# Optimization experiments

Measured on AMD Instinct MI355X. Metric: run time of the kernel, lower is better.

Reference implementation:

```python
import jax, jax.numpy as jnp
import numpy as np

MIN_NORM = 1e-15
EPS = 1e-7     # float32 eps used by the Hyperboloid manifold
MAX_NORM = 1e6

# ---- Hyperboloid (Lorentz) math, curvature c = k > 0, K = 1/k ----

def mink_dot(x, y):
    return jnp.sum(x * y, -1, keepdims=True) - 2.0 * x[..., :1] * y[..., :1]

def mink_norm(u):
    return jnp.sqrt(jnp.clip(mink_dot(u, u), EPS, None))

def proj(x, k):
    # project onto hyperboloid: x0 = sqrt(K + ||y||^2), spatial part kept
    K = 1.0 / k
    y = x[..., 1:]
    x0 = jnp.sqrt(jnp.clip(K + jnp.sum(y * y, -1, keepdims=True), EPS, None))
    return jnp.concatenate([x0, y], -1)

def proj_tan(u, x, k):
    ux = jnp.sum(x[..., 1:] * u[..., 1:], -1, keepdims=True)
    u0 = ux / jnp.clip(x[..., :1], EPS, None)
    return jnp.concatenate([u0 * jnp.ones_like(u[..., :1]), u[..., 1:]], -1)

def expmap(u, x, k):
    sqrtK = jnp.sqrt(1.0 / k)
    theta = jnp.clip(jnp.clip(mink_norm(u), None, MAX_NORM) / sqrtK, MIN_NORM, None)
    return proj(jnp.cosh(theta) * x + jnp.sinh(theta) * u / theta, k)

def expmap0(u, k):
    sqrtK = jnp.sqrt(1.0 / k)
    s = u[..., 1:]
    sn = jnp.clip(jnp.linalg.norm(s, axis=-1, keepdims=True), MIN_NORM, None)
    theta = sn / sqrtK
    out = jnp.concatenate([sqrtK * jnp.cosh(theta), sqrtK * jnp.sinh(theta) * s / sn], -1)
    return proj(out, k)

def logmap0(x, k):
    sqrtK = jnp.sqrt(1.0 / k)
    y = x[..., 1:]
    yn = jnp.clip(jnp.linalg.norm(y, axis=-1, keepdims=True), MIN_NORM, None)
    theta = jnp.clip(x[..., :1] / sqrtK, 1.0 + EPS, None)
    sp = sqrtK * jnp.arccosh(theta) * y / yn
    return jnp.concatenate([jnp.zeros_like(sp[..., :1]), sp], -1)

def ptransp0(x, u, k):
    sqrtK = jnp.sqrt(1.0 / k)
    x0, y = x[..., :1], x[..., 1:]
    yn = jnp.clip(jnp.linalg.norm(y, axis=-1, keepdims=True), MIN_NORM, None)
    yh = y / yn
    v = jnp.concatenate([-yn, (sqrtK - x0) * yh], -1)
    alpha = jnp.sum(yh * u[..., 1:], -1, keepdims=True) / sqrtK
    return proj_tan(u - alpha * v, x, k)

def mobius_matvec(m, x, k):
    return expmap0(logmap0(x, k) @ m.T, k)

def mobius_add(x, y, k):
    return expmap(ptransp0(x, logmap0(y, k), k), x, k)

def one_rnn_transform(W, h, U, x, b, k):
    Wh_Ux = mobius_add(mobius_matvec(W, h, k), mobius_matvec(U, x, k), k)
    return mobius_add(Wh_Ux, expmap0(b, k), k)

# ---- Mobius GRU cell (hyperbolic_hidden_state0=True, hyperbolic_input=False,
#      hyperbolic_output=True, nonlin=None) ----

def gru_cell(xt, hx, weight_ih, weight_hh, bias, k):
    # prepend zero time-coordinate and lift Euclidean input onto the hyperboloid
    xt = jnp.concatenate([jnp.zeros_like(xt[..., :1]), xt], -1)
    xt = expmap0(xt, k)
    W_ir, W_ih, W_iz = jnp.split(weight_ih, 3, axis=0)
    W_hr, W_hh, W_hz = jnp.split(weight_hh, 3, axis=0)
    b_r, b_h, b_z = bias[0:1], bias[1:2], bias[2:3]
    z_t = jax.nn.sigmoid(logmap0(one_rnn_transform(W_hz, hx, W_iz, xt, b_z, k), k))
    r_t = jax.nn.sigmoid(logmap0(one_rnn_transform(W_hr, hx, W_ir, xt, b_r, k), k))
    rh_t = expmap0(r_t * logmap0(hx, k), k)
    h_tilde = one_rnn_transform(W_hh, rh_t, W_ih, xt, b_h, k)
    delta_h = mobius_add(proj(-hx, k), h_tilde, k)
    h_int = ptransp0(hx, z_t * logmap0(delta_h, k), k)
    return expmap(h_int, hx, k)  # hyperbolic_output=True -> no final logmap0


def setup_inputs() -> dict:
    key = jax.random.key(0)
    k0, k1, k2, k3 = jax.random.split(key, 4)
    B, T, Din, H = 64, 512, 256, 256
    H1, D1 = H + 1, Din + 1
    stdv = 1.0 / np.sqrt(H1)
    x = 0.1 * jax.random.normal(k0, (B, T, Din), jnp.float32)
    weight_ih = jax.random.uniform(k1, (3 * H1, D1), jnp.float32, -stdv, stdv)
    weight_hh = jax.random.uniform(k2, (3 * H1, H1), jnp.float32, -stdv, stdv)
    bias = jnp.concatenate(
        [jnp.zeros((3, 1), jnp.float32), 1e-5 * jax.random.normal(k3, (3, H), jnp.float32)], -1)
    kk = jnp.ones((1,), jnp.float32)
    return {"x": x, "k": kk, "weight_ih": weight_ih, "weight_hh": weight_hh, "bias": bias}


def reference(x, k, weight_ih, weight_hh, bias):
    B = x.shape[0]
    H1 = weight_hh.shape[1]
    h0 = jnp.zeros((B, H1), x.dtype)  # default h0 (num_layers = 1)
    x_tm = jnp.swapaxes(x, 0, 1)  # [T, B, Din]

    def step(hx, xt):
        h = gru_cell(xt, hx, weight_ih, weight_hh, bias, k)
        return h, h

    h_last, outs = jax.lax.scan(step, h0, x_tm)  # outs: [T, B, H1]
    ht = h_last[..., 1:][None]  # drop time coord -> [1, B, H]
    return outs, ht
```

## Files before the change

### kernel.cpp

```cpp
#include <hip/hip_runtime.h>
#include <hip/hip_fp16.h>
#include <stdint.h>

#define B_  64
#define T_  512
#define H1_ 257

typedef _Float16 h2v __attribute__((ext_vector_type(2)));

__device__ __forceinline__ float frcp(float x) { return __builtin_amdgcn_rcpf(x); }
__device__ __forceinline__ float frsq(float x) { return __builtin_amdgcn_rsqf(x); }
__device__ __forceinline__ h2v u2h(uint32_t u) { return __builtin_bit_cast(h2v, u); }
__device__ __forceinline__ float fdot2(uint32_t a, uint32_t b, float c) {
  return __builtin_amdgcn_fdot2(u2h(a), u2h(b), c, false);
}
__device__ __forceinline__ uint32_t pkh(float a, float b) {
  __half2 h = __halves2half2(__float2half(a), __float2half(b));
  return __builtin_bit_cast(uint32_t, h);
}

#define LDS_BAR() do { \
  asm volatile("s_waitcnt lgkmcnt(0)" ::: "memory"); \
  __builtin_amdgcn_s_barrier(); \
  asm volatile("" ::: "memory"); \
} while (0)

template <int CTRL>
__device__ __forceinline__ float dpp_add(float v) {
  int t = __builtin_amdgcn_update_dpp(0, __builtin_bit_cast(int, v), CTRL, 0xf, 0xf, true);
  return v + __builtin_bit_cast(float, t);
}
__device__ __forceinline__ float wsum(float v) {
  v = dpp_add<0xB1>(v);  v = dpp_add<0x4E>(v);
  v = dpp_add<0x141>(v); v = dpp_add<0x140>(v);
  v = dpp_add<0x142>(v); v = dpp_add<0x143>(v);
  return __builtin_bit_cast(float, __builtin_amdgcn_readlane(__builtin_bit_cast(int, v), 63));
}
__device__ __forceinline__ void wsum2(float a, float b, float& ra, float& rb) {
  a = dpp_add<0xB1>(a);  b = dpp_add<0xB1>(b);
  a = dpp_add<0x4E>(a);  b = dpp_add<0x4E>(b);
  a = dpp_add<0x141>(a); b = dpp_add<0x141>(b);
  a = dpp_add<0x140>(a); b = dpp_add<0x140>(b);
  a = dpp_add<0x142>(a); b = dpp_add<0x142>(b);
  a = dpp_add<0x143>(a); b = dpp_add<0x143>(b);
  ra = __builtin_bit_cast(float, __builtin_amdgcn_readlane(__builtin_bit_cast(int, a), 63));
  rb = __builtin_bit_cast(float, __builtin_amdgcn_readlane(__builtin_bit_cast(int, b), 63));
}
__device__ __forceinline__ float sq4w(const float* s) {
  return wsum(s[0]*s[0] + s[1]*s[1] + s[2]*s[2] + s[3]*s[3]);
}
__device__ __forceinline__ float dot4w(const float* a, const float* b) {
  return wsum(a[0]*b[0] + a[1]*b[1] + a[2]*b[2] + a[3]*b[3]);
}

__device__ __forceinline__ float logc_(float x0, float ss, float sqrtK, float rsqK) {
  float yn = sqrtf(fmaxf(ss, 1e-30f));
  float th = fmaxf(x0 * rsqK, 1.0f + 1e-7f);
  float ac = __logf(th + sqrtf(th*th - 1.0f));
  return sqrtK * ac * frcp(yn);
}

__device__ __forceinline__ void madd_body(float* xs, float ss, float x0,
                                          const float* lm, float ssl, float dotXL,
                                          float K, float sqrtK, float rsqK) {
  float inv = frsq(fmaxf(ss, 1e-30f));
  float alpha = inv * dotXL * rsqK;
  float c2 = alpha * (sqrtK - x0);
  float ciw = c2 * inv;
  float ux = dotXL - ciw * ss;
  float w0 = ux * frcp(fmaxf(x0, 1e-7f));
  float ssw = fmaxf(ssl - 2.0f*ciw*dotXL + ciw*ciw*ss, 0.0f);
  float md = ssw - w0 * w0;
  float mn = sqrtf(fmaxf(md, 1e-7f));
  float th = fmaxf(fminf(mn, 1e6f) * rsqK, 1e-15f);
  float ex = __expf(th), ei = frcp(ex);
  float ch = 0.5f * (ex + ei);
  float sh = 0.5f * (ex - ei) * frcp(th);
  float A = ch - sh * ciw;
#pragma unroll
  for (int e = 0; e < 4; ++e) xs[e] = A * xs[e] + sh * lm[e];
}

__device__ __forceinline__ float madds_body(float* xs, float ss, float x0,
                                            const float* lm, float ssl, float dotXL,
                                            float sqrtK, float rsqK) {
  float inv = frsq(fmaxf(ss, 1e-30f));
  float alpha = inv * dotXL * rsqK;
  float c2 = alpha * (sqrtK - x0);
  float ciw = c2 * inv;
  float ux = dotXL - ciw * ss;
  float ssw = fmaxf(ssl - 2.0f*ciw*dotXL + ciw*ciw*ss, 0.0f);
  float nss = fmaxf(ss + 2.0f*ux + ssw, 0.0f);
  float Bc = 1.0f - ciw;
#pragma unroll
  for (int e = 0; e < 4; ++e) xs[e] = Bc * xs[e] + lm[e];
  return nss;
}

__device__ __forceinline__ void gate_chain(float* v, const float* lq, float ssl_q,
                                           const float* lmb, float ssl_b,
                                           float K, float sqrtK, float rsqK, float* sig) {
  float ssv, dvl;
  wsum2(v[0]*v[0]+v[1]*v[1]+v[2]*v[2]+v[3]*v[3],
        v[0]*lq[0]+v[1]*lq[1]+v[2]*lq[2]+v[3]*lq[3], ssv, dvl);
  float sn = sqrtf(fmaxf(ssv, 1e-30f));
  float th = sn * rsqK;
  float ex = __expf(th), ei = frcp(ex);
  float sh = 0.5f * (ex - ei);
  float ce = sqrtK * sh * frcp(sn);
#pragma unroll
  for (int e = 0; e < 4; ++e) v[e] = ce * v[e];
  float tq = sqrtK * sh;
  float ss = tq * tq;
  float x0 = sqrtf(fmaxf(K + ss, 1e-7f));
  madd_body(v, ss, x0, lq, ssl_q, ce * dvl, K, sqrtK, rsqK);
  float ssm, dbm;
  wsum2(v[0]*v[0]+v[1]*v[1]+v[2]*v[2]+v[3]*v[3],
        v[0]*lmb[0]+v[1]*lmb[1]+v[2]*lmb[2]+v[3]*lmb[3], ssm, dbm);
  float x0m = sqrtf(fmaxf(K + ssm, 1e-7f));
  float nss = madds_body(v, ssm, x0m, lmb, ssl_b, dbm, sqrtK, rsqK);
  float x0f = sqrtf(fmaxf(K + nss, 1e-7f));
  float c = logc_(x0f, nss, sqrtK, rsqK);
#pragma unroll
  for (int e = 0; e < 4; ++e) sig[e] = frcp(1.0f + __expf(-c * v[e]));
}

__global__ void pack_weights(const float* __restrict__ wih, const float* __restrict__ whh,
                             uint4* __restrict__ Pih, uint4* __restrict__ Phh) {
  int idx = blockIdx.x * 256 + threadIdx.x;
  int m   = idx / 24576;
  int rem = idx % 24576;
  int k4  = rem / 768;
  int col = rem % 768;
  int g   = col >> 8;
  int j   = col & 255;
  int gsrc = (g == 0) ? 2 : ((g == 1) ? 0 : 1);
  const float* src = (m == 0) ? wih : whh;
  const float* row = src + (size_t)(gsrc * H1_ + 1 + j) * H1_ + 1 + 8 * k4;
  uint4 o;
  o.x = pkh(row[0], row[1]);
  o.y = pkh(row[2], row[3]);
  o.z = pkh(row[4], row[5]);
  o.w = pkh(row[6], row[7]);
  ((m == 0) ? Pih : Phh)[(size_t)k4 * 768 + col] = o;
}

__global__ void precompute_xu(const float* __restrict__ x, const uint4* __restrict__ U4,
                              float* __restrict__ xU) {
  __shared__ __align__(16) uint32_t xp[8][128];
  const int tid = threadIdx.x;
  const int row0 = blockIdx.x * 8;
#pragma unroll
  for (int it = 0; it < 4; ++it) {
    int item = it * 256 + tid;
    int r = item >> 7, i = item & 127;
    int row = row0 + r;
    int t = row >> 6, bb = row & 63;
    const float* xr = x + ((size_t)bb * T_ + t) * 256;
    float2 xv = ((const float2*)xr)[i];
    xp[r][i] = pkh(xv.x, xv.y);
  }
  __syncthreads();
  float acc[8][3];
#pragma unroll
  for (int r = 0; r < 8; ++r)
#pragma unroll
    for (int c = 0; c < 3; ++c) acc[r][c] = 0.f;

#pragma unroll 2
  for (int k4 = 0; k4 < 32; ++k4) {
    uint4 w0 = U4[(size_t)k4 * 768 + tid];
    uint4 w1 = U4[(size_t)k4 * 768 + 256 + tid];
    uint4 w2 = U4[(size_t)k4 * 768 + 512 + tid];
#pragma unroll
    for (int r = 0; r < 8; ++r) {
      uint4 gp = ((const uint4*)xp[r])[k4];
      acc[r][0] = fdot2(w0.x, gp.x, acc[r][0]); acc[r][0] = fdot2(w0.y, gp.y, acc[r][0]);
      acc[r][0] = fdot2(w0.z, gp.z, acc[r][0]); acc[r][0] = fdot2(w0.w, gp.w, acc[r][0]);
      acc[r][1] = fdot2(w1.x, gp.x, acc[r][1]); acc[r][1] = fdot2(w1.y, gp.y, acc[r][1]);
      acc[r][1] = fdot2(w1.z, gp.z, acc[r][1]); acc[r][1] = fdot2(w1.w, gp.w, acc[r][1]);
      acc[r][2] = fdot2(w2.x, gp.x, acc[r][2]); acc[r][2] = fdot2(w2.y, gp.y, acc[r][2]);
      acc[r][2] = fdot2(w2.z, gp.z, acc[r][2]); acc[r][2] = fdot2(w2.w, gp.w, acc[r][2]);
    }
  }
#pragma unroll
  for (int r = 0; r < 8; ++r)
#pragma unroll
    for (int c = 0; c < 3; ++c)
      xU[(size_t)(row0 + r) * 768 + c * 256 + tid] = acc[r][c];
}

__global__ void xuss_kernel(const float* __restrict__ xU, float* __restrict__ xUss) {
  int row  = (blockIdx.x * 256 + threadIdx.x) >> 6;
  int lane = threadIdx.x & 63;
  const float4* base = (const float4*)(xU + (size_t)row * 768);
#pragma unroll
  for (int g = 0; g < 3; ++g) {
    float4 v = base[g * 64 + lane];
    float s = wsum(v.x*v.x + v.y*v.y + v.z*v.z + v.w*v.w);
    if (lane == 63) xUss[(size_t)row * 3 + g] = s;
  }
}

__global__ __launch_bounds__(512, 1) void mobius_gru_scan(
    const float* __restrict__ xU, const float* __restrict__ xUss,
    const uint4* __restrict__ W4, const float* __restrict__ bias,
    const float* __restrict__ kin, float* __restrict__ out) {
  __shared__ __align__(16) uint4 LWH[32][256];
  __shared__ __align__(16) uint32_t lds_gp[128];
  __shared__ __align__(16) float lds_v[512];
  __shared__ __align__(16) float lds_v2[512];
  __shared__ __align__(16) float lds_vh[512];
  __shared__ __align__(16) float lds_zg[256];

  const int tid  = threadIdx.x;
  const int lane = tid & 63;
  const int wave = tid >> 6;
  const int b    = blockIdx.x;
  const int j    = tid & 255;
  const int kh   = tid >> 8;

  const float kk    = kin[0];
  const float K     = 1.0f / kk;
  const float sqrtK = sqrtf(K);
  const float rsqK  = 1.0f / sqrtK;

#pragma unroll
  for (int it = 0; it < 16; ++it) {
    int idx = it * 512 + tid;
    int k4 = idx >> 8, jj = idx & 255;
    LWH[k4][jj] = W4[(size_t)k4 * 768 + 512 + jj];
  }

  uint4 vz[16], vr[16];
#pragma unroll
  for (int i = 0; i < 16; ++i) vz[i] = W4[(size_t)(kh * 16 + i) * 768 + j];
#pragma unroll
  for (int i = 0; i < 16; ++i) vr[i] = W4[(size_t)(kh * 16 + i) * 768 + 256 + j];
#pragma unroll
  for (int i = 0; i < 16; ++i) {
    asm volatile("" : "+v"(vz[i].x), "+v"(vz[i].y), "+v"(vz[i].z), "+v"(vz[i].w));
    asm volatile("" : "+v"(vr[i].x), "+v"(vr[i].y), "+v"(vr[i].z), "+v"(vr[i].w));
  }

  float lmeb[3][4]; float sslb[3];
  {
    const int rows[3] = {2, 0, 1};
#pragma unroll
    for (int g = 0; g < 3; ++g) {
#pragma unroll
      for (int e = 0; e < 4; ++e) lmeb[g][e] = bias[rows[g] * H1_ + 1 + 4 * lane + e];
      sslb[g] = sq4w(lmeb[g]);
    }
  }

  float h0c = 0.f, hs[4] = {0.f, 0.f, 0.f, 0.f}, ssh = 0.f;
  float gh[4] = {0.f, 0.f, 0.f, 0.f};

  float4 xvr_c = {0,0,0,0}, xvh_c = {0,0,0,0}, xvz_c = {0,0,0,0};
  float s0c = 0.f, s1c = 0.f, s2c = 0.f;
  if (wave == 0) {
    const float* xrow = xU + (size_t)b * 768;
    xvr_c = ((const float4*)(xrow + 256))[lane];
    xvh_c = ((const float4*)(xrow + 512))[lane];
    const float* srow = xUss + (size_t)b * 3;
    s1c = srow[1]; s2c = srow[2];
    uint2 p; p.x = 0u; p.y = 0u;
    ((uint2*)lds_gp)[lane] = p;
  } else if (wave == 1) {
    const float* xrow = xU + (size_t)b * 768;
    xvz_c = ((const float4*)xrow)[lane];
    s0c = xUss[(size_t)b * 3];
  }

  __syncthreads();

  for (int t = 0; t < T_; ++t) {
    if (t) LDS_BAR();

    {
      float a0 = 0.f, a1 = 0.f, a2 = 0.f, a3 = 0.f;
      float c0 = 0.f, c1 = 0.f, c2 = 0.f, c3 = 0.f;
#pragma unroll
      for (int i = 0; i < 16; ++i) {
        uint4 gp = ((const uint4*)lds_gp)[kh * 16 + i];
        a0 = fdot2(vr[i].x, gp.x, a0);
        a1 = fdot2(vr[i].y, gp.y, a1);
        a2 = fdot2(vr[i].z, gp.z, a2);
        a3 = fdot2(vr[i].w, gp.w, a3);
        c0 = fdot2(vz[i].x, gp.x, c0);
        c1 = fdot2(vz[i].y, gp.y, c1);
        c2 = fdot2(vz[i].z, gp.z, c2);
        c3 = fdot2(vz[i].w, gp.w, c3);
      }
      lds_v[kh * 256 + j]  = (a0 + a1) + (a2 + a3);
      lds_v2[kh * 256 + j] = (c0 + c1) + (c2 + c3);
    }
    float4 xvr_n = {0,0,0,0}, xvh_n = {0,0,0,0}, xvz_n = {0,0,0,0};
    float s0n = 0.f, s1n = 0.f, s2n = 0.f;
    if (t + 1 < T_) {
      if (wave == 0) {
        const float* nx = xU + (size_t)((t + 1) * B_ + b) * 768;
        xvr_n = ((const float4*)(nx + 256))[lane];
        xvh_n = ((const float4*)(nx + 512))[lane];
        const float* srow = xUss + (size_t)((t + 1) * B_ + b) * 3;
        s1n = srow[1]; s2n = srow[2];
      } else if (wave == 1) {
        const float* nx = xU + (size_t)((t + 1) * B_ + b) * 768;
        xvz_n = ((const float4*)nx)[lane];
        s0n = xUss[(size_t)((t + 1) * B_ + b) * 3];
      }
    }
    LDS_BAR();

    if (wave == 0) {
      float v[4], xv[4];
      {
        float4 pa = ((const float4*)lds_v)[lane];
        float4 pb = ((const float4*)lds_v)[64 + lane];
        v[0] = pa.x + pb.x; v[1] = pa.y + pb.y; v[2] = pa.z + pb.z; v[3] = pa.w + pb.w;
      }
      xv[0] = xvr_c.x; xv[1] = xvr_c.y; xv[2] = xvr_c.z; xv[3] = xvr_c.w;
      float rg[4];
      gate_chain(v, xv, s1c, lmeb[1], sslb[1], K, sqrtK, rsqK, rg);
      uint2 p;
      p.x = pkh(rg[0] * gh[0], rg[1] * gh[1]);
      p.y = pkh(rg[2] * gh[2], rg[3] * gh[3]);
      ((uint2*)lds_gp)[lane] = p;
    } else if (wave == 1) {
      float v[4], xv[4];
      {
        float4 pa = ((const float4*)lds_v2)[lane];
        float4 pb = ((const float4*)lds_v2)[64 + lane];
        v[0] = pa.x + pb.x; v[1] = pa.y + pb.y; v[2] = pa.z + pb.z; v[3] = pa.w + pb.w;
      }
      xv[0] = xvz_c.x; xv[1] = xvz_c.y; xv[2] = xvz_c.z; xv[3] = xvz_c.w;
      float zg[4];
      gate_chain(v, xv, s0c, lmeb[0], sslb[0], K, sqrtK, rsqK, zg);
      float4 z4 = {zg[0], zg[1], zg[2], zg[3]};
      ((float4*)lds_zg)[lane] = z4;
    }
    LDS_BAR();

    {
      const uint4* wl = &LWH[kh * 16][j];
      float a0 = 0.f, a1 = 0.f, a2 = 0.f, a3 = 0.f;
#pragma unroll
      for (int i = 0; i < 16; ++i) {
        uint4 w  = wl[(size_t)i * 256];
        uint4 gp = ((const uint4*)lds_gp)[kh * 16 + i];
        a0 = fdot2(w.x, gp.x, a0);
        a1 = fdot2(w.y, gp.y, a1);
        a2 = fdot2(w.z, gp.z, a2);
        a3 = fdot2(w.w, gp.w, a3);
      }
      lds_vh[kh * 256 + j] = (a0 + a1) + (a2 + a3);
    }
    LDS_BAR();

    if (wave == 0) {
      float4 z4 = ((const float4*)lds_zg)[lane];
      float4 pa = ((const float4*)lds_vh)[lane];
      float4 pb = ((const float4*)lds_vh)[64 + lane];

      float ts[4] = {pa.x + pb.x, pa.y + pb.y, pa.z + pb.z, pa.w + pb.w};
      float xv[4] = {xvh_c.x, xvh_c.y, xvh_c.z, xvh_c.w};
      float ssv, dvl;
      wsum2(ts[0]*ts[0]+ts[1]*ts[1]+ts[2]*ts[2]+ts[3]*ts[3],
            ts[0]*xv[0]+ts[1]*xv[1]+ts[2]*xv[2]+ts[3]*xv[3], ssv, dvl);
      float sn = sqrtf(fmaxf(ssv, 1e-30f));
      float th = sn * rsqK;
      float ex = __expf(th), ei = frcp(ex);
      float shh = 0.5f * (ex - ei);
      float ce = sqrtK * shh * frcp(sn);
#pragma unroll
      for (int e = 0; e < 4; ++e) ts[e] = ce * ts[e];
      float tq = sqrtK * shh;
      float sse = tq * tq;
      float x0e = sqrtf(fmaxf(K + sse, 1e-7f));
      madd_body(ts, sse, x0e, xv, s2c, ce * dvl, K, sqrtK, rsqK);
      float sst, dbm;
      wsum2(ts[0]*ts[0]+ts[1]*ts[1]+ts[2]*ts[2]+ts[3]*ts[3],
            ts[0]*lmeb[2][0]+ts[1]*lmeb[2][1]+ts[2]*lmeb[2][2]+ts[3]*lmeb[2][3],
            sst, dbm);
      float x0t = sqrtf(fmaxf(K + sst, 1e-7f));
      float nst = madds_body(ts, sst, x0t, lmeb[2], sslb[2], dbm, sqrtK, rsqK);
      float t0 = sqrtf(fmaxf(K + nst, 1e-7f));

      float ynt = sqrtf(fmaxf(nst, 1e-30f));
      float tht = fmaxf(t0 * rsqK, 1.0f + 1e-7f);
      float act = __logf(tht + sqrtf(tht*tht - 1.0f));
      float clt = sqrtK * act * frcp(ynt);
      float lt[4];
#pragma unroll
      for (int e = 0; e < 4; ++e) lt[e] = clt * ts[e];
      float sslt = K * act * act;

      float ns[4] = {-hs[0], -hs[1], -hs[2], -hs[3]};
      float n0 = sqrtf(fmaxf(K + ssh, 1e-7f));
      float dnl = dot4w(ns, lt);
      madd_body(ns, ssh, n0, lt, sslt, dnl, K, sqrtK, rsqK);
      float ssn2 = sq4w(ns);
      float n02 = sqrtf(fmaxf(K + ssn2, 1e-7f));
      float cl2 = logc_(n02, ssn2, sqrtK, rsqK);

      float uu[4];
      uu[0] = z4.x * (cl2 * ns[0]); uu[1] = z4.y * (cl2 * ns[1]);
      uu[2] = z4.z * (cl2 * ns[2]); uu[3] = z4.w * (cl2 * ns[3]);
      float ssuu, dhu;
      wsum2(uu[0]*uu[0]+uu[1]*uu[1]+uu[2]*uu[2]+uu[3]*uu[3],
            hs[0]*uu[0]+hs[1]*uu[1]+hs[2]*uu[2]+hs[3]*uu[3], ssuu, dhu);
      madd_body(hs, ssh, h0c, uu, ssuu, dhu, K, sqrtK, rsqK);
      ssh = sq4w(hs);
      h0c = sqrtf(fmaxf(K + ssh, 1e-7f));

      float cg = logc_(h0c, ssh, sqrtK, rsqK);
#pragma unroll
      for (int e = 0; e < 4; ++e) gh[e] = cg * hs[e];
      uint2 p; p.x = pkh(gh[0], gh[1]); p.y = pkh(gh[2], gh[3]);
      ((uint2*)lds_gp)[lane] = p;

      float* orow = out + (size_t)(t * B_ + b) * H1_;
      if (lane == 0) orow[0] = h0c;
#pragma unroll
      for (int e = 0; e < 4; ++e) orow[1 + 4 * lane + e] = hs[e];
    }

    xvr_c = xvr_n; xvh_c = xvh_n; xvz_c = xvz_n;
    s0c = s0n; s1c = s1n; s2c = s2n;
  }

  if (wave == 0) {
    float4 hv = {hs[0], hs[1], hs[2], hs[3]};
    ((float4*)(out + (size_t)T_ * B_ * H1_ + (size_t)b * 256))[lane] = hv;
  }
}

extern "C" void kernel_launch(void* const* d_in, const int* in_sizes, int n_in,
                              void* d_out, int out_size, void* d_ws, size_t ws_size,
                              hipStream_t stream) {
  const float* x    = (const float*)d_in[0];
  const float* k    = (const float*)d_in[1];
  const float* wih  = (const float*)d_in[2];
  const float* whh  = (const float*)d_in[3];
  const float* bias = (const float*)d_in[4];
  float* out = (float*)d_out;

  uint4* Pih = (uint4*)d_ws;
  uint4* Phh = Pih + 24576;
  float* xU  = (float*)(Phh + 24576);
  float* xUss = (float*)Pih;

  pack_weights<<<192, 256, 0, stream>>>(wih, whh, Pih, Phh);
  precompute_xu<<<4096, 256, 0, stream>>>(x, Pih, xU);
  xuss_kernel<<<8192, 256, 0, stream>>>(xU, xUss);
  mobius_gru_scan<<<B_, 512, 0, stream>>>(xU, xUss, Phh, bias, k, out);
}
```

Measured before the change: 1.952 ms.

## Process two batch rows per scan block to reuse register and LDS weights

```diff
diff --git a/kernel.cpp b/kernel.cpp
--- a/kernel.cpp
+++ b/kernel.cpp
@@ -207,18 +207,20 @@
     const uint4* __restrict__ W4, const float* __restrict__ bias,
     const float* __restrict__ kin, float* __restrict__ out) {
   __shared__ __align__(16) uint4 LWH[32][256];
-  __shared__ __align__(16) uint32_t lds_gp[128];
-  __shared__ __align__(16) float lds_v[512];
-  __shared__ __align__(16) float lds_v2[512];
-  __shared__ __align__(16) float lds_vh[512];
-  __shared__ __align__(16) float lds_zg[256];
+  __shared__ __align__(16) uint32_t lds_gp[2][128];
+  __shared__ __align__(16) float lds_v[2][512];
+  __shared__ __align__(16) float lds_v2[2][512];
+  __shared__ __align__(16) float lds_vh[2][512];
+  __shared__ __align__(16) float lds_zg[2][256];
 
   const int tid  = threadIdx.x;
   const int lane = tid & 63;
   const int wave = tid >> 6;
-  const int b    = blockIdx.x;
+  const int b0   = blockIdx.x * 2;
   const int j    = tid & 255;
   const int kh   = tid >> 8;
+  const int mrow = (wave >> 1) & 1;
+  const int mb   = b0 + mrow;
 
   const float kk    = kin[0];
   const float K     = 1.0f / kk;
@@ -259,18 +261,18 @@
 
   float4 xvr_c = {0,0,0,0}, xvh_c = {0,0,0,0}, xvz_c = {0,0,0,0};
   float s0c = 0.f, s1c = 0.f, s2c = 0.f;
-  if (wave == 0) {
-    const float* xrow = xU + (size_t)b * 768;
+  if (wave == 0 || wave == 2) {
+    const float* xrow = xU + (size_t)mb * 768;
     xvr_c = ((const float4*)(xrow + 256))[lane];
     xvh_c = ((const float4*)(xrow + 512))[lane];
-    const float* srow = xUss + (size_t)b * 3;
+    const float* srow = xUss + (size_t)mb * 3;
     s1c = srow[1]; s2c = srow[2];
     uint2 p; p.x = 0u; p.y = 0u;
-    ((uint2*)lds_gp)[lane] = p;
-  } else if (wave == 1) {
-    const float* xrow = xU + (size_t)b * 768;
+    ((uint2*)lds_gp[mrow])[lane] = p;
+  } else if (wave == 1 || wave == 3) {
+    const float* xrow = xU + (size_t)mb * 768;
     xvz_c = ((const float4*)xrow)[lane];
-    s0c = xUss[(size_t)b * 3];
+    s0c = xUss[(size_t)mb * 3];
   }
 
   __syncthreads();
@@ -281,43 +283,48 @@
     {
       float a0 = 0.f, a1 = 0.f, a2 = 0.f, a3 = 0.f;
       float c0 = 0.f, c1 = 0.f, c2 = 0.f, c3 = 0.f;
+      float d0 = 0.f, d1 = 0.f, d2 = 0.f, d3 = 0.f;
+      float e0 = 0.f, e1 = 0.f, e2 = 0.f, e3 = 0.f;
 #pragma unroll
       for (int i = 0; i < 16; ++i) {
-        uint4 gp = ((const uint4*)lds_gp)[kh * 16 + i];
-        a0 = fdot2(vr[i].x, gp.x, a0);
-        a1 = fdot2(vr[i].y, gp.y, a1);
-        a2 = fdot2(vr[i].z, gp.z, a2);
-        a3 = fdot2(vr[i].w, gp.w, a3);
-        c0 = fdot2(vz[i].x, gp.x, c0);
-        c1 = fdot2(vz[i].y, gp.y, c1);
-        c2 = fdot2(vz[i].z, gp.z, c2);
-        c3 = fdot2(vz[i].w, gp.w, c3);
+        uint4 g0 = ((const uint4*)lds_gp[0])[kh * 16 + i];
+        uint4 g1 = ((const uint4*)lds_gp[1])[kh * 16 + i];
+        a0 = fdot2(vr[i].x, g0.x, a0); a1 = fdot2(vr[i].y, g0.y, a1);
+        a2 = fdot2(vr[i].z, g0.z, a2); a3 = fdot2(vr[i].w, g0.w, a3);
+        c0 = fdot2(vz[i].x, g0.x, c0); c1 = fdot2(vz[i].y, g0.y, c1);
+        c2 = fdot2(vz[i].z, g0.z, c2); c3 = fdot2(vz[i].w, g0.w, c3);
+        d0 = fdot2(vr[i].x, g1.x, d0); d1 = fdot2(vr[i].y, g1.y, d1);
+        d2 = fdot2(vr[i].z, g1.z, d2); d3 = fdot2(vr[i].w, g1.w, d3);
+        e0 = fdot2(vz[i].x, g1.x, e0); e1 = fdot2(vz[i].y, g1.y, e1);
+        e2 = fdot2(vz[i].z, g1.z, e2); e3 = fdot2(vz[i].w, g1.w, e3);
       }
-      lds_v[kh * 256 + j]  = (a0 + a1) + (a2 + a3);
-      lds_v2[kh * 256 + j] = (c0 + c1) + (c2 + c3);
+      lds_v[0][kh * 256 + j]  = (a0 + a1) + (a2 + a3);
+      lds_v2[0][kh * 256 + j] = (c0 + c1) + (c2 + c3);
+      lds_v[1][kh * 256 + j]  = (d0 + d1) + (d2 + d3);
+      lds_v2[1][kh * 256 + j] = (e0 + e1) + (e2 + e3);
     }
     float4 xvr_n = {0,0,0,0}, xvh_n = {0,0,0,0}, xvz_n = {0,0,0,0};
     float s0n = 0.f, s1n = 0.f, s2n = 0.f;
     if (t + 1 < T_) {
-      if (wave == 0) {
-        const float* nx = xU + (size_t)((t + 1) * B_ + b) * 768;
+      if (wave == 0 || wave == 2) {
+        const float* nx = xU + (size_t)((t + 1) * B_ + mb) * 768;
         xvr_n = ((const float4*)(nx + 256))[lane];
         xvh_n = ((const float4*)(nx + 512))[lane];
-        const float* srow = xUss + (size_t)((t + 1) * B_ + b) * 3;
+        const float* srow = xUss + (size_t)((t + 1) * B_ + mb) * 3;
         s1n = srow[1]; s2n = srow[2];
-      } else if (wave == 1) {
-        const float* nx = xU + (size_t)((t + 1) * B_ + b) * 768;
+      } else if (wave == 1 || wave == 3) {
+        const float* nx = xU + (size_t)((t + 1) * B_ + mb) * 768;
         xvz_n = ((const float4*)nx)[lane];
-        s0n = xUss[(size_t)((t + 1) * B_ + b) * 3];
+        s0n = xUss[(size_t)((t + 1) * B_ + mb) * 3];
       }
     }
     LDS_BAR();
 
-    if (wave == 0) {
+    if (wave == 0 || wave == 2) {
       float v[4], xv[4];
       {
-        float4 pa = ((const float4*)lds_v)[lane];
-        float4 pb = ((const float4*)lds_v)[64 + lane];
+        float4 pa = ((const float4*)lds_v[mrow])[lane];
+        float4 pb = ((const float4*)lds_v[mrow])[64 + lane];
         v[0] = pa.x + pb.x; v[1] = pa.y + pb.y; v[2] = pa.z + pb.z; v[3] = pa.w + pb.w;
       }
       xv[0] = xvr_c.x; xv[1] = xvr_c.y; xv[2] = xvr_c.z; xv[3] = xvr_c.w;
@@ -326,42 +333,45 @@
       uint2 p;
       p.x = pkh(rg[0] * gh[0], rg[1] * gh[1]);
       p.y = pkh(rg[2] * gh[2], rg[3] * gh[3]);
-      ((uint2*)lds_gp)[lane] = p;
-    } else if (wave == 1) {
+      ((uint2*)lds_gp[mrow])[lane] = p;
+    } else if (wave == 1 || wave == 3) {
       float v[4], xv[4];
       {
-        float4 pa = ((const float4*)lds_v2)[lane];
-        float4 pb = ((const float4*)lds_v2)[64 + lane];
+        float4 pa = ((const float4*)lds_v2[mrow])[lane];
+        float4 pb = ((const float4*)lds_v2[mrow])[64 + lane];
         v[0] = pa.x + pb.x; v[1] = pa.y + pb.y; v[2] = pa.z + pb.z; v[3] = pa.w + pb.w;
       }
       xv[0] = xvz_c.x; xv[1] = xvz_c.y; xv[2] = xvz_c.z; xv[3] = xvz_c.w;
       float zg[4];
       gate_chain(v, xv, s0c, lmeb[0], sslb[0], K, sqrtK, rsqK, zg);
       float4 z4 = {zg[0], zg[1], zg[2], zg[3]};
-      ((float4*)lds_zg)[lane] = z4;
+      ((float4*)lds_zg[mrow])[lane] = z4;
     }
     LDS_BAR();
 
     {
       const uint4* wl = &LWH[kh * 16][j];
       float a0 = 0.f, a1 = 0.f, a2 = 0.f, a3 = 0.f;
+      float d0 = 0.f, d1 = 0.f, d2 = 0.f, d3 = 0.f;
 #pragma unroll
       for (int i = 0; i < 16; ++i) {
         uint4 w  = wl[(size_t)i * 256];
-        uint4 gp = ((const uint4*)lds_gp)[kh * 16 + i];
-        a0 = fdot2(w.x, gp.x, a0);
-        a1 = fdot2(w.y, gp.y, a1);
-        a2 = fdot2(w.z, gp.z, a2);
-        a3 = fdot2(w.w, gp.w, a3);
+        uint4 g0 = ((const uint4*)lds_gp[0])[kh * 16 + i];
+        uint4 g1 = ((const uint4*)lds_gp[1])[kh * 16 + i];
+        a0 = fdot2(w.x, g0.x, a0); a1 = fdot2(w.y, g0.y, a1);
+        a2 = fdot2(w.z, g0.z, a2); a3 = fdot2(w.w, g0.w, a3);
+        d0 = fdot2(w.x, g1.x, d0); d1 = fdot2(w.y, g1.y, d1);
+        d2 = fdot2(w.z, g1.z, d2); d3 = fdot2(w.w, g1.w, d3);
       }
-      lds_vh[kh * 256 + j] = (a0 + a1) + (a2 + a3);
+      lds_vh[0][kh * 256 + j] = (a0 + a1) + (a2 + a3);
+      lds_vh[1][kh * 256 + j] = (d0 + d1) + (d2 + d3);
     }
     LDS_BAR();
 
-    if (wave == 0) {
-      float4 z4 = ((const float4*)lds_zg)[lane];
-      float4 pa = ((const float4*)lds_vh)[lane];
-      float4 pb = ((const float4*)lds_vh)[64 + lane];
+    if (wave == 0 || wave == 2) {
+      float4 z4 = ((const float4*)lds_zg[mrow])[lane];
+      float4 pa = ((const float4*)lds_vh[mrow])[lane];
+      float4 pb = ((const float4*)lds_vh[mrow])[64 + lane];
 
       float ts[4] = {pa.x + pb.x, pa.y + pb.y, pa.z + pb.z, pa.w + pb.w};
       float xv[4] = {xvh_c.x, xvh_c.y, xvh_c.z, xvh_c.w};
@@ -418,9 +428,9 @@
 #pragma unroll
       for (int e = 0; e < 4; ++e) gh[e] = cg * hs[e];
       uint2 p; p.x = pkh(gh[0], gh[1]); p.y = pkh(gh[2], gh[3]);
-      ((uint2*)lds_gp)[lane] = p;
-
-      float* orow = out + (size_t)(t * B_ + b) * H1_;
+      ((uint2*)lds_gp[mrow])[lane] = p;
+
+      float* orow = out + (size_t)(t * B_ + mb) * H1_;
       if (lane == 0) orow[0] = h0c;
 #pragma unroll
       for (int e = 0; e < 4; ++e) orow[1 + 4 * lane + e] = hs[e];
@@ -430,9 +440,9 @@
     s0c = s0n; s1c = s1n; s2c = s2n;
   }
 
-  if (wave == 0) {
+  if (wave == 0 || wave == 2) {
     float4 hv = {hs[0], hs[1], hs[2], hs[3]};
-    ((float4*)(out + (size_t)T_ * B_ * H1_ + (size_t)b * 256))[lane] = hv;
+    ((float4*)(out + (size_t)T_ * B_ * H1_ + (size_t)mb * 256))[lane] = hv;
   }
 }
 
@@ -454,5 +464,5 @@
   pack_weights<<<192, 256, 0, stream>>>(wih, whh, Pih, Phh);
   precompute_xu<<<4096, 256, 0, stream>>>(x, Pih, xU);
   xuss_kernel<<<8192, 256, 0, stream>>>(xU, xUss);
-  mobius_gru_scan<<<B_, 512, 0, stream>>>(xU, xUss, Phh, bias, k, out);
-}
+  mobius_gru_scan<<<B_ / 2, 512, 0, stream>>>(xU, xUss, Phh, bias, k, out);
+}
```

Result: slower. 2.417 ms (+23.8%).

## Fold dot-product reduction into earlier wave sums and prefetch hidden weights

Applied to the files above, without the earlier changes.

```diff
diff --git a/kernel.cpp b/kernel.cpp
--- a/kernel.cpp
+++ b/kernel.cpp
@@ -46,11 +46,20 @@
   ra = __builtin_bit_cast(float, __builtin_amdgcn_readlane(__builtin_bit_cast(int, a), 63));
   rb = __builtin_bit_cast(float, __builtin_amdgcn_readlane(__builtin_bit_cast(int, b), 63));
 }
+__device__ __forceinline__ void wsum3(float a, float b, float c,
+                                      float& ra, float& rb, float& rc) {
+  a = dpp_add<0xB1>(a);  b = dpp_add<0xB1>(b);  c = dpp_add<0xB1>(c);
+  a = dpp_add<0x4E>(a);  b = dpp_add<0x4E>(b);  c = dpp_add<0x4E>(c);
+  a = dpp_add<0x141>(a); b = dpp_add<0x141>(b); c = dpp_add<0x141>(c);
+  a = dpp_add<0x140>(a); b = dpp_add<0x140>(b); c = dpp_add<0x140>(c);
+  a = dpp_add<0x142>(a); b = dpp_add<0x142>(b); c = dpp_add<0x142>(c);
+  a = dpp_add<0x143>(a); b = dpp_add<0x143>(b); c = dpp_add<0x143>(c);
+  ra = __builtin_bit_cast(float, __builtin_amdgcn_readlane(__builtin_bit_cast(int, a), 63));
+  rb = __builtin_bit_cast(float, __builtin_amdgcn_readlane(__builtin_bit_cast(int, b), 63));
+  rc = __builtin_bit_cast(float, __builtin_amdgcn_readlane(__builtin_bit_cast(int, c), 63));
+}
 __device__ __forceinline__ float sq4w(const float* s) {
   return wsum(s[0]*s[0] + s[1]*s[1] + s[2]*s[2] + s[3]*s[3]);
-}
-__device__ __forceinline__ float dot4w(const float* a, const float* b) {
-  return wsum(a[0]*b[0] + a[1]*b[1] + a[2]*b[2] + a[3]*b[3]);
 }
 
 __device__ __forceinline__ float logc_(float x0, float ss, float sqrtK, float rsqK) {
@@ -83,7 +92,7 @@
 
 __device__ __forceinline__ float madds_body(float* xs, float ss, float x0,
                                             const float* lm, float ssl, float dotXL,
-                                            float sqrtK, float rsqK) {
+                                            float sqrtK, float rsqK, float& Bc_out) {
   float inv = frsq(fmaxf(ss, 1e-30f));
   float alpha = inv * dotXL * rsqK;
   float c2 = alpha * (sqrtK - x0);
@@ -92,6 +101,7 @@
   float ssw = fmaxf(ssl - 2.0f*ciw*dotXL + ciw*ciw*ss, 0.0f);
   float nss = fmaxf(ss + 2.0f*ux + ssw, 0.0f);
   float Bc = 1.0f - ciw;
+  Bc_out = Bc;
 #pragma unroll
   for (int e = 0; e < 4; ++e) xs[e] = Bc * xs[e] + lm[e];
   return nss;
@@ -118,7 +128,8 @@
   wsum2(v[0]*v[0]+v[1]*v[1]+v[2]*v[2]+v[3]*v[3],
         v[0]*lmb[0]+v[1]*lmb[1]+v[2]*lmb[2]+v[3]*lmb[3], ssm, dbm);
   float x0m = sqrtf(fmaxf(K + ssm, 1e-7f));
-  float nss = madds_body(v, ssm, x0m, lmb, ssl_b, dbm, sqrtK, rsqK);
+  float Bc;
+  float nss = madds_body(v, ssm, x0m, lmb, ssl_b, dbm, sqrtK, rsqK, Bc);
   float x0f = sqrtf(fmaxf(K + nss, 1e-7f));
   float c = logc_(x0f, nss, sqrtK, rsqK);
 #pragma unroll
@@ -312,6 +323,13 @@
       }
     }
     LDS_BAR();
+
+    uint4 wpre[16];
+    {
+      const uint4* wl = &LWH[kh * 16][j];
+#pragma unroll
+      for (int i = 0; i < 16; ++i) wpre[i] = wl[(size_t)i * 256];
+    }
 
     if (wave == 0) {
       float v[4], xv[4];
@@ -343,16 +361,14 @@
     LDS_BAR();
 
     {
-      const uint4* wl = &LWH[kh * 16][j];
       float a0 = 0.f, a1 = 0.f, a2 = 0.f, a3 = 0.f;
 #pragma unroll
       for (int i = 0; i < 16; ++i) {
-        uint4 w  = wl[(size_t)i * 256];
         uint4 gp = ((const uint4*)lds_gp)[kh * 16 + i];
-        a0 = fdot2(w.x, gp.x, a0);
-        a1 = fdot2(w.y, gp.y, a1);
-        a2 = fdot2(w.z, gp.z, a2);
-        a3 = fdot2(w.w, gp.w, a3);
+        a0 = fdot2(wpre[i].x, gp.x, a0);
+        a1 = fdot2(wpre[i].y, gp.y, a1);
+        a2 = fdot2(wpre[i].z, gp.z, a2);
+        a3 = fdot2(wpre[i].w, gp.w, a3);
       }
       lds_vh[kh * 256 + j] = (a0 + a1) + (a2 + a3);
     }
@@ -365,9 +381,11 @@
 
       float ts[4] = {pa.x + pb.x, pa.y + pb.y, pa.z + pb.z, pa.w + pb.w};
       float xv[4] = {xvh_c.x, xvh_c.y, xvh_c.z, xvh_c.w};
-      float ssv, dvl;
-      wsum2(ts[0]*ts[0]+ts[1]*ts[1]+ts[2]*ts[2]+ts[3]*ts[3],
-            ts[0]*xv[0]+ts[1]*xv[1]+ts[2]*xv[2]+ts[3]*xv[3], ssv, dvl);
+      float ssv, dvl, dhb;
+      wsum3(ts[0]*ts[0]+ts[1]*ts[1]+ts[2]*ts[2]+ts[3]*ts[3],
+            ts[0]*xv[0]+ts[1]*xv[1]+ts[2]*xv[2]+ts[3]*xv[3],
+            hs[0]*lmeb[2][0]+hs[1]*lmeb[2][1]+hs[2]*lmeb[2][2]+hs[3]*lmeb[2][3],
+            ssv, dvl, dhb);
       float sn = sqrtf(fmaxf(ssv, 1e-30f));
       float th = sn * rsqK;
       float ex = __expf(th), ei = frcp(ex);
@@ -379,12 +397,14 @@
       float sse = tq * tq;
       float x0e = sqrtf(fmaxf(K + sse, 1e-7f));
       madd_body(ts, sse, x0e, xv, s2c, ce * dvl, K, sqrtK, rsqK);
-      float sst, dbm;
-      wsum2(ts[0]*ts[0]+ts[1]*ts[1]+ts[2]*ts[2]+ts[3]*ts[3],
+      float sst, dbm, dnt;
+      wsum3(ts[0]*ts[0]+ts[1]*ts[1]+ts[2]*ts[2]+ts[3]*ts[3],
             ts[0]*lmeb[2][0]+ts[1]*lmeb[2][1]+ts[2]*lmeb[2][2]+ts[3]*lmeb[2][3],
-            sst, dbm);
+            hs[0]*ts[0]+hs[1]*ts[1]+hs[2]*ts[2]+hs[3]*ts[3],
+            sst, dbm, dnt);
       float x0t = sqrtf(fmaxf(K + sst, 1e-7f));
-      float nst = madds_body(ts, sst, x0t, lmeb[2], sslb[2], dbm, sqrtK, rsqK);
+      float Bc;
+      float nst = madds_body(ts, sst, x0t, lmeb[2], sslb[2], dbm, sqrtK, rsqK, Bc);
       float t0 = sqrtf(fmaxf(K + nst, 1e-7f));
 
       float ynt = sqrtf(fmaxf(nst, 1e-30f));
@@ -395,10 +415,10 @@
 #pragma unroll
       for (int e = 0; e < 4; ++e) lt[e] = clt * ts[e];
       float sslt = K * act * act;
+      float dnl = -(clt * (Bc * dnt + dhb));
 
       float ns[4] = {-hs[0], -hs[1], -hs[2], -hs[3]};
       float n0 = sqrtf(fmaxf(K + ssh, 1e-7f));
-      float dnl = dot4w(ns, lt);
       madd_body(ns, ssh, n0, lt, sslt, dnl, K, sqrtK, rsqK);
       float ssn2 = sq4w(ns);
       float n02 = sqrtf(fmaxf(K + ssn2, 1e-7f));
```

Result: slower. 3.033 ms (+55.4%).
